# Performance work log

Measured on AMD Instinct MI355X. Metric: run time of the kernel, lower is better.

## Reference

```python
import jax, jax.numpy as jnp
import numpy as np

N, K = 100000, 16
XN_IN, XE_IN, XN_OUT = 128, 64, 128
STDV = 0.01


def setup_inputs() -> dict:
    key = jax.random.key(0)
    k1, k2, k3, k4, k5, k6 = jax.random.split(key, 6)
    x = jax.random.normal(k1, (N, XN_IN), dtype=jnp.float32)
    e = jax.random.normal(k2, (N, K, XE_IN), dtype=jnp.float32)
    ij = jax.random.randint(k3, (N, K, 2), 0, N, dtype=jnp.int64)
    Wc = jax.random.normal(k4, (XN_OUT, XN_IN), dtype=jnp.float32) * STDV
    Wn = jax.random.normal(k5, (XN_OUT, XN_IN), dtype=jnp.float32) * STDV
    We = jax.random.normal(k6, (XN_OUT, XE_IN), dtype=jnp.float32) * STDV
    return {"x": x, "e": e, "ij": ij, "Wc": Wc, "Wn": Wn, "We": We}


def reference(x, e, ij, Wc, Wn, We):
    # neighbor indices: column 0 of last dim, shape [N, K]
    nh = ij[:, :, 0]
    # mean-pool neighbor node features: [N, K, xn_in] -> [N, xn_in]
    xnj = jnp.mean(x[nh], axis=1)
    # mean-pool incident edge features: [N, K, xe_in] -> [N, xe_in]
    xej = jnp.mean(e, axis=1)
    # fused batched matvecs: Wc@xi + Wn@xnj + We@xej, per node
    out = x @ Wc.T + xnj @ Wn.T + xej @ We.T
    return jax.nn.relu(out)
```

## Files before the change

kernel.cpp:

```cpp
#include <hip/hip_runtime.h>

#define N_ROWS 100000
#define KNB 16
#define XN 128
#define XE 64
#define XO 128
#define KA 320
#define AP 328
#define MT 16
#define NTILES (N_ROWS / MT)
#define GRID_MAIN 2048

typedef __attribute__((ext_vector_type(8))) short bf16x8_t;
typedef __attribute__((ext_vector_type(4))) float f32x4_t;

__device__ __forceinline__ short f2bf(float f) {
  union { float f; unsigned u; } v; v.f = f;
  unsigned r = v.u + 0x7fffu + ((v.u >> 16) & 1u);
  return (short)(r >> 16);
}

__global__ void detect_idx_kernel(const int* __restrict__ ij32, int* __restrict__ flag) {
  if (threadIdx.x == 0 && blockIdx.x == 0) {
    int all0 = 1;
    for (int i = 0; i < 16; ++i) all0 &= (ij32[2 * i + 1] == 0) ? 1 : 0;
    *flag = all0;
  }
}

__global__ __launch_bounds__(256, 3) void conv_fused_kernel(
    const float* __restrict__ x, const float* __restrict__ e,
    const int* __restrict__ ij32,
    const float* __restrict__ Wc, const float* __restrict__ Wn,
    const float* __restrict__ We,
    const int* __restrict__ flag, float* __restrict__ out)
{
  __shared__ short As[MT][AP];
  __shared__ int nhs[MT * KNB];

  const int tid  = threadIdx.x;
  const int wave = tid >> 6;
  const int lane = tid & 63;
  const int quad = lane >> 4;
  const int l16  = lane & 15;
  const int r16  = tid >> 4;
  const int s16  = tid & 15;

  const int shift = (*flag) ? 2 : 1;

  bf16x8_t bfrag[2][10];
  #pragma unroll
  for (int t = 0; t < 2; ++t) {
    const int col = wave * 32 + t * 16 + l16;
    #pragma unroll
    for (int ks = 0; ks < 10; ++ks) {
      const int k = ks * 32 + quad * 8;
      const float* src;
      if (k < 128)      src = Wc + col * XN + k;
      else if (k < 256) src = Wn + col * XN + (k - 128);
      else              src = We + col * XE + (k - 256);
      float4 a = *(const float4*)src;
      float4 b = *(const float4*)(src + 4);
      bf16x8_t f;
      f[0] = f2bf(a.x); f[1] = f2bf(a.y); f[2] = f2bf(a.z); f[3] = f2bf(a.w);
      f[4] = f2bf(b.x); f[5] = f2bf(b.y); f[6] = f2bf(b.z); f[7] = f2bf(b.w);
      bfrag[t][ks] = f;
    }
  }

  for (int tile = blockIdx.x; tile < NTILES; tile += gridDim.x) {
    const int r0 = tile * MT;
    __syncthreads();

    nhs[tid] = ij32[((r0 + r16) * KNB + s16) << shift];

    {
      const float* p = x + (r0 + r16) * XN + s16 * 8;
      float4 a = *(const float4*)p;
      float4 b = *(const float4*)(p + 4);
      short* dst = &As[r16][s16 * 8];
      dst[0] = f2bf(a.x); dst[1] = f2bf(a.y); dst[2] = f2bf(a.z); dst[3] = f2bf(a.w);
      dst[4] = f2bf(b.x); dst[5] = f2bf(b.y); dst[6] = f2bf(b.z); dst[7] = f2bf(b.w);
    }
    {
      const float* p = e + (r0 + r16) * (KNB * XE) + s16 * 4;
      float sx = 0.f, sy = 0.f, sz = 0.f, sw = 0.f;
      #pragma unroll 4
      for (int k = 0; k < KNB; ++k) {
        float4 v = *(const float4*)(p + k * XE);
        sx += v.x; sy += v.y; sz += v.z; sw += v.w;
      }
      short* dst = &As[r16][256 + s16 * 4];
      dst[0] = f2bf(sx * 0.0625f); dst[1] = f2bf(sy * 0.0625f);
      dst[2] = f2bf(sz * 0.0625f); dst[3] = f2bf(sw * 0.0625f);
    }
    __syncthreads();
    {
      float s0=0,s1=0,s2=0,s3=0,s4=0,s5=0,s6=0,s7=0;
      #pragma unroll 4
      for (int k = 0; k < KNB; ++k) {
        int idx = nhs[r16 * KNB + k];
        idx = idx < 0 ? 0 : (idx >= N_ROWS ? N_ROWS - 1 : idx);
        const float* p = x + idx * XN + s16 * 8;
        float4 a = *(const float4*)p;
        float4 b = *(const float4*)(p + 4);
        s0 += a.x; s1 += a.y; s2 += a.z; s3 += a.w;
        s4 += b.x; s5 += b.y; s6 += b.z; s7 += b.w;
      }
      short* dst = &As[r16][128 + s16 * 8];
      dst[0] = f2bf(s0 * 0.0625f); dst[1] = f2bf(s1 * 0.0625f);
      dst[2] = f2bf(s2 * 0.0625f); dst[3] = f2bf(s3 * 0.0625f);
      dst[4] = f2bf(s4 * 0.0625f); dst[5] = f2bf(s5 * 0.0625f);
      dst[6] = f2bf(s6 * 0.0625f); dst[7] = f2bf(s7 * 0.0625f);
    }
    __syncthreads();

    f32x4_t acc0 = {0.f, 0.f, 0.f, 0.f};
    f32x4_t acc1 = {0.f, 0.f, 0.f, 0.f};
    #pragma unroll
    for (int ks = 0; ks < 10; ++ks) {
      bf16x8_t af = *(const bf16x8_t*)(&As[l16][ks * 32 + quad * 8]);
      acc0 = __builtin_amdgcn_mfma_f32_16x16x32_bf16(af, bfrag[0][ks], acc0, 0, 0, 0);
      acc1 = __builtin_amdgcn_mfma_f32_16x16x32_bf16(af, bfrag[1][ks], acc1, 0, 0, 0);
    }

    const int colb = wave * 32 + l16;
    #pragma unroll
    for (int i = 0; i < 4; ++i) {
      const int row = r0 + quad * 4 + i;
      out[row * XO + colb]      = fmaxf(acc0[i], 0.f);
      out[row * XO + colb + 16] = fmaxf(acc1[i], 0.f);
    }
  }
}

extern "C" void kernel_launch(void* const* d_in, const int* in_sizes, int n_in,
                              void* d_out, int out_size, void* d_ws, size_t ws_size,
                              hipStream_t stream) {
  const float* x  = (const float*)d_in[0];
  const float* e  = (const float*)d_in[1];
  const int* ij32 = (const int*)d_in[2];
  const float* Wc = (const float*)d_in[3];
  const float* Wn = (const float*)d_in[4];
  const float* We = (const float*)d_in[5];
  float* out = (float*)d_out;
  int* flag = (int*)d_ws;

  detect_idx_kernel<<<1, 64, 0, stream>>>(ij32, flag);
  conv_fused_kernel<<<GRID_MAIN, 256, 0, stream>>>(x, e, ij32, Wc, Wn, We, flag, out);
}
```

Baseline: 661.9 us.

## Pre-cast x and weights to bf16, gather neighbors in bf16, one tile per block

Adds a cast kernel that converts x and the three weight matrices to bf16 in workspace, so the neighbor gather reads half the bytes per row. The main kernel drops the persistent grid-stride loop and launches one 32-row tile per 512-thread block, with neighbor indices broadcast by wave shuffles instead of shared memory. It also uses nontemporal loads and stores for streaming e, ij and out. The trade-offs are an extra full pass over x, an extra launch, per-block reloading of the weight fragments, and a fallback fp32 path when the workspace is too small.

```diff
diff --git a/kernel.cpp b/kernel.cpp
--- a/kernel.cpp
+++ b/kernel.cpp
@@ -5,11 +5,10 @@
 #define XN 128
 #define XE 64
 #define XO 128
-#define KA 320
 #define AP 328
-#define MT 16
+#define MT 32
 #define NTILES (N_ROWS / MT)
-#define GRID_MAIN 2048
+#define TPB 512
 
 typedef __attribute__((ext_vector_type(8))) short bf16x8_t;
 typedef __attribute__((ext_vector_type(4))) float f32x4_t;
@@ -18,6 +17,11 @@
   union { float f; unsigned u; } v; v.f = f;
   unsigned r = v.u + 0x7fffu + ((v.u >> 16) & 1u);
   return (short)(r >> 16);
+}
+__device__ __forceinline__ float bf2f(short s) {
+  union { unsigned u; float f; } v;
+  v.u = ((unsigned)(unsigned short)s) << 16;
+  return v.f;
 }
 
 __global__ void detect_idx_kernel(const int* __restrict__ ij32, int* __restrict__ flag) {
@@ -28,109 +32,147 @@
   }
 }
 
-__global__ __launch_bounds__(256, 3) void conv_fused_kernel(
-    const float* __restrict__ x, const float* __restrict__ e,
-    const int* __restrict__ ij32,
+#define XCH  (N_ROWS * XN / 8)
+#define WCCH (XO * XN / 8)
+#define WECH (XO * XE / 8)
+__global__ __launch_bounds__(256) void cast_kernel(
+    const float* __restrict__ x, const float* __restrict__ Wc,
+    const float* __restrict__ Wn, const float* __restrict__ We,
+    short* __restrict__ xb, short* __restrict__ wb) {
+  const int total = XCH + 2 * WCCH + WECH;
+  for (int i = blockIdx.x * blockDim.x + threadIdx.x; i < total;
+       i += gridDim.x * blockDim.x) {
+    const float* s; short* d;
+    if (i < XCH) { s = x + (size_t)i * 8; d = xb + (size_t)i * 8; }
+    else {
+      int j = i - XCH;
+      if (j < WCCH)          { s = Wc + j * 8;              d = wb + j * 8; }
+      else if (j < 2 * WCCH) { s = Wn + (j - WCCH) * 8;     d = wb + XO * XN + (j - WCCH) * 8; }
+      else                   { s = We + (j - 2 * WCCH) * 8; d = wb + 2 * XO * XN + (j - 2 * WCCH) * 8; }
+    }
+    f32x4_t a = __builtin_nontemporal_load((const f32x4_t*)s);
+    f32x4_t b = __builtin_nontemporal_load((const f32x4_t*)s + 1);
+    bf16x8_t r;
+    r[0] = f2bf(a[0]); r[1] = f2bf(a[1]); r[2] = f2bf(a[2]); r[3] = f2bf(a[3]);
+    r[4] = f2bf(b[0]); r[5] = f2bf(b[1]); r[6] = f2bf(b[2]); r[7] = f2bf(b[3]);
+    *(bf16x8_t*)d = r;
+  }
+}
+
+template<bool XB>
+__global__ __launch_bounds__(TPB, 4) void conv_fused_kernel(
+    const float* __restrict__ x, const short* __restrict__ xb,
+    const float* __restrict__ e, const int* __restrict__ ij32,
     const float* __restrict__ Wc, const float* __restrict__ Wn,
-    const float* __restrict__ We,
+    const float* __restrict__ We, const short* __restrict__ wb,
     const int* __restrict__ flag, float* __restrict__ out)
 {
-  __shared__ short As[MT][AP];
-  __shared__ int nhs[MT * KNB];
+  __shared__ __align__(16) short As[MT][AP];
 
   const int tid  = threadIdx.x;
   const int wave = tid >> 6;
   const int lane = tid & 63;
   const int quad = lane >> 4;
   const int l16  = lane & 15;
-  const int r16  = tid >> 4;
+  const int r    = tid >> 4;
   const int s16  = tid & 15;
 
   const int shift = (*flag) ? 2 : 1;
-
-  bf16x8_t bfrag[2][10];
+  const int r0 = blockIdx.x * MT;
+
+  int myidx = __builtin_nontemporal_load(ij32 + (((r0 + r) * KNB + s16) << shift));
+  myidx = myidx < 0 ? 0 : (myidx >= N_ROWS ? N_ROWS - 1 : myidx);
+
+  if constexpr (XB) {
+    *(bf16x8_t*)(&As[r][s16 * 8]) = *(const bf16x8_t*)(xb + (r0 + r) * XN + s16 * 8);
+  } else {
+    const float* p = x + (r0 + r) * XN + s16 * 8;
+    f32x4_t a = *(const f32x4_t*)p;
+    f32x4_t b = *(const f32x4_t*)(p + 4);
+    short* dst = &As[r][s16 * 8];
+    dst[0] = f2bf(a[0]); dst[1] = f2bf(a[1]); dst[2] = f2bf(a[2]); dst[3] = f2bf(a[3]);
+    dst[4] = f2bf(b[0]); dst[5] = f2bf(b[1]); dst[6] = f2bf(b[2]); dst[7] = f2bf(b[3]);
+  }
+
+  {
+    float s0=0,s1=0,s2=0,s3=0,s4=0,s5=0,s6=0,s7=0;
+    #pragma unroll
+    for (int k = 0; k < KNB; ++k) {
+      const int idx = __shfl(myidx, (lane & 48) | k, 64);
+      if constexpr (XB) {
+        bf16x8_t v = *(const bf16x8_t*)(xb + idx * XN + s16 * 8);
+        s0 += bf2f(v[0]); s1 += bf2f(v[1]); s2 += bf2f(v[2]); s3 += bf2f(v[3]);
+        s4 += bf2f(v[4]); s5 += bf2f(v[5]); s6 += bf2f(v[6]); s7 += bf2f(v[7]);
+      } else {
+        const float* p = x + idx * XN + s16 * 8;
+        f32x4_t a = *(const f32x4_t*)p;
+        f32x4_t b = *(const f32x4_t*)(p + 4);
+        s0 += a[0]; s1 += a[1]; s2 += a[2]; s3 += a[3];
+        s4 += b[0]; s5 += b[1]; s6 += b[2]; s7 += b[3];
+      }
+    }
+    short* dst = &As[r][128 + s16 * 8];
+    dst[0] = f2bf(s0 * 0.0625f); dst[1] = f2bf(s1 * 0.0625f);
+    dst[2] = f2bf(s2 * 0.0625f); dst[3] = f2bf(s3 * 0.0625f);
+    dst[4] = f2bf(s4 * 0.0625f); dst[5] = f2bf(s5 * 0.0625f);
+    dst[6] = f2bf(s6 * 0.0625f); dst[7] = f2bf(s7 * 0.0625f);
+  }
+
+  {
+    const float* p = e + (size_t)(r0 + r) * (KNB * XE) + s16 * 4;
+    float sx = 0.f, sy = 0.f, sz = 0.f, sw = 0.f;
+    #pragma unroll
+    for (int k = 0; k < KNB; ++k) {
+      f32x4_t v = __builtin_nontemporal_load((const f32x4_t*)(p + k * XE));
+      sx += v[0]; sy += v[1]; sz += v[2]; sw += v[3];
+    }
+    short* dst = &As[r][256 + s16 * 4];
+    dst[0] = f2bf(sx * 0.0625f); dst[1] = f2bf(sy * 0.0625f);
+    dst[2] = f2bf(sz * 0.0625f); dst[3] = f2bf(sw * 0.0625f);
+  }
+
+  bf16x8_t bfrag[10];
+  const int col = wave * 16 + l16;
   #pragma unroll
-  for (int t = 0; t < 2; ++t) {
-    const int col = wave * 32 + t * 16 + l16;
-    #pragma unroll
-    for (int ks = 0; ks < 10; ++ks) {
-      const int k = ks * 32 + quad * 8;
+  for (int ks = 0; ks < 10; ++ks) {
+    const int k = ks * 32 + quad * 8;
+    if constexpr (XB) {
+      const short* src;
+      if (k < 128)      src = wb + col * XN + k;
+      else if (k < 256) src = wb + XO * XN + col * XN + (k - 128);
+      else              src = wb + 2 * XO * XN + col * XE + (k - 256);
+      bfrag[ks] = *(const bf16x8_t*)src;
+    } else {
       const float* src;
       if (k < 128)      src = Wc + col * XN + k;
       else if (k < 256) src = Wn + col * XN + (k - 128);
       else              src = We + col * XE + (k - 256);
-      float4 a = *(const float4*)src;
-      float4 b = *(const float4*)(src + 4);
+      f32x4_t a = *(const f32x4_t*)src;
+      f32x4_t b = *(const f32x4_t*)(src + 4);
       bf16x8_t f;
-      f[0] = f2bf(a.x); f[1] = f2bf(a.y); f[2] = f2bf(a.z); f[3] = f2bf(a.w);
-      f[4] = f2bf(b.x); f[5] = f2bf(b.y); f[6] = f2bf(b.z); f[7] = f2bf(b.w);
-      bfrag[t][ks] = f;
-    }
-  }
-
-  for (int tile = blockIdx.x; tile < NTILES; tile += gridDim.x) {
-    const int r0 = tile * MT;
-    __syncthreads();
-
-    nhs[tid] = ij32[((r0 + r16) * KNB + s16) << shift];
-
-    {
-      const float* p = x + (r0 + r16) * XN + s16 * 8;
-      float4 a = *(const float4*)p;
-      float4 b = *(const float4*)(p + 4);
-      short* dst = &As[r16][s16 * 8];
-      dst[0] = f2bf(a.x); dst[1] = f2bf(a.y); dst[2] = f2bf(a.z); dst[3] = f2bf(a.w);
-      dst[4] = f2bf(b.x); dst[5] = f2bf(b.y); dst[6] = f2bf(b.z); dst[7] = f2bf(b.w);
-    }
-    {
-      const float* p = e + (r0 + r16) * (KNB * XE) + s16 * 4;
-      float sx = 0.f, sy = 0.f, sz = 0.f, sw = 0.f;
-      #pragma unroll 4
-      for (int k = 0; k < KNB; ++k) {
-        float4 v = *(const float4*)(p + k * XE);
-        sx += v.x; sy += v.y; sz += v.z; sw += v.w;
-      }
-      short* dst = &As[r16][256 + s16 * 4];
-      dst[0] = f2bf(sx * 0.0625f); dst[1] = f2bf(sy * 0.0625f);
-      dst[2] = f2bf(sz * 0.0625f); dst[3] = f2bf(sw * 0.0625f);
-    }
-    __syncthreads();
-    {
-      float s0=0,s1=0,s2=0,s3=0,s4=0,s5=0,s6=0,s7=0;
-      #pragma unroll 4
-      for (int k = 0; k < KNB; ++k) {
-        int idx = nhs[r16 * KNB + k];
-        idx = idx < 0 ? 0 : (idx >= N_ROWS ? N_ROWS - 1 : idx);
-        const float* p = x + idx * XN + s16 * 8;
-        float4 a = *(const float4*)p;
-        float4 b = *(const float4*)(p + 4);
-        s0 += a.x; s1 += a.y; s2 += a.z; s3 += a.w;
-        s4 += b.x; s5 += b.y; s6 += b.z; s7 += b.w;
-      }
-      short* dst = &As[r16][128 + s16 * 8];
-      dst[0] = f2bf(s0 * 0.0625f); dst[1] = f2bf(s1 * 0.0625f);
-      dst[2] = f2bf(s2 * 0.0625f); dst[3] = f2bf(s3 * 0.0625f);
-      dst[4] = f2bf(s4 * 0.0625f); dst[5] = f2bf(s5 * 0.0625f);
-      dst[6] = f2bf(s6 * 0.0625f); dst[7] = f2bf(s7 * 0.0625f);
-    }
-    __syncthreads();
-
-    f32x4_t acc0 = {0.f, 0.f, 0.f, 0.f};
-    f32x4_t acc1 = {0.f, 0.f, 0.f, 0.f};
-    #pragma unroll
-    for (int ks = 0; ks < 10; ++ks) {
-      bf16x8_t af = *(const bf16x8_t*)(&As[l16][ks * 32 + quad * 8]);
-      acc0 = __builtin_amdgcn_mfma_f32_16x16x32_bf16(af, bfrag[0][ks], acc0, 0, 0, 0);
-      acc1 = __builtin_amdgcn_mfma_f32_16x16x32_bf16(af, bfrag[1][ks], acc1, 0, 0, 0);
-    }
-
-    const int colb = wave * 32 + l16;
-    #pragma unroll
-    for (int i = 0; i < 4; ++i) {
-      const int row = r0 + quad * 4 + i;
-      out[row * XO + colb]      = fmaxf(acc0[i], 0.f);
-      out[row * XO + colb + 16] = fmaxf(acc1[i], 0.f);
-    }
+      f[0] = f2bf(a[0]); f[1] = f2bf(a[1]); f[2] = f2bf(a[2]); f[3] = f2bf(a[3]);
+      f[4] = f2bf(b[0]); f[5] = f2bf(b[1]); f[6] = f2bf(b[2]); f[7] = f2bf(b[3]);
+      bfrag[ks] = f;
+    }
+  }
+
+  __syncthreads();
+
+  f32x4_t acc0 = {0.f, 0.f, 0.f, 0.f};
+  f32x4_t acc1 = {0.f, 0.f, 0.f, 0.f};
+  #pragma unroll
+  for (int ks = 0; ks < 10; ++ks) {
+    bf16x8_t a0 = *(const bf16x8_t*)(&As[l16][ks * 32 + quad * 8]);
+    bf16x8_t a1 = *(const bf16x8_t*)(&As[l16 + 16][ks * 32 + quad * 8]);
+    acc0 = __builtin_amdgcn_mfma_f32_16x16x32_bf16(a0, bfrag[ks], acc0, 0, 0, 0);
+    acc1 = __builtin_amdgcn_mfma_f32_16x16x32_bf16(a1, bfrag[ks], acc1, 0, 0, 0);
+  }
+
+  #pragma unroll
+  for (int i = 0; i < 4; ++i) {
+    const int row0 = r0 + quad * 4 + i;
+    __builtin_nontemporal_store(fmaxf(acc0[i], 0.f), out + row0 * XO + col);
+    __builtin_nontemporal_store(fmaxf(acc1[i], 0.f), out + (row0 + 16) * XO + col);
   }
 }
 
@@ -144,8 +186,22 @@
   const float* Wn = (const float*)d_in[4];
   const float* We = (const float*)d_in[5];
   float* out = (float*)d_out;
+
   int* flag = (int*)d_ws;
+  const size_t xb_off   = 256;
+  const size_t xb_elems = (size_t)N_ROWS * XN;
+  const size_t wb_elems = (size_t)(2 * XO * XN + XO * XE);
+  const size_t need     = xb_off + (xb_elems + wb_elems) * sizeof(short);
 
   detect_idx_kernel<<<1, 64, 0, stream>>>(ij32, flag);
-  conv_fused_kernel<<<GRID_MAIN, 256, 0, stream>>>(x, e, ij32, Wc, Wn, We, flag, out);
-}
+  if (ws_size >= need) {
+    short* xb = (short*)((char*)d_ws + xb_off);
+    short* wb = xb + xb_elems;
+    cast_kernel<<<2048, 256, 0, stream>>>(x, Wc, Wn, We, xb, wb);
+    conv_fused_kernel<true><<<NTILES, TPB, 0, stream>>>(
+        x, xb, e, ij32, Wc, Wn, We, wb, flag, out);
+  } else {
+    conv_fused_kernel<false><<<NTILES, TPB, 0, stream>>>(
+        x, nullptr, e, ij32, Wc, Wn, We, nullptr, flag, out);
+  }
+}
```

New measurement: 602.7 us. 8.9% less time.
